# Performance work log

Hardware: AMD Instinct MI355X
Metric: run time of the kernel (lower is better)

Reference implementation:

```python
import jax, jax.numpy as jnp
import numpy as np

NUM_HEADS = 8
GRAPH_DIM = 64
K_RATIO = 0.1
SIM_THRESH = 0.6


def _gat_layer(h_in, mask, W, a_src, a_dst, b):
    # PyG GATConv (heads=1, eval mode): lin (no bias), alpha = LeakyReLU(a_src.h_j + a_dst.h_i),
    # softmax over source nodes j per target i (edges given by dense mask, self loops included), + bias.
    h = h_in @ W                                   # [N, F]
    asrc = h @ a_src                               # [N] source term
    adst = h @ a_dst                               # [N] target term
    logits = jax.nn.leaky_relu(adst[:, None] + asrc[None, :], 0.2)  # [target i, source j]
    logits = jnp.where(mask.T, logits, -1e30)      # mask[j,i]: edge src j -> dst i (symmetric here)
    alpha = jax.nn.softmax(logits, axis=-1)
    return alpha @ h + b


def _forward(x, w_qkv, w_proj, b_proj, gat0_W, gat0_asrc, gat0_adst, gat0_b,
             gat1_W, gat1_asrc, gat1_adst, gat1_b, w_g2a, b_g2a):
    B, C, H, W = x.shape
    HW = H * W
    nh = NUM_HEADS
    hd = C // nh
    scale = hd ** -0.5
    x_seq = x.reshape(B, C, HW).transpose(0, 2, 1)                 # [B, HW, C]

    # ---- build_spatial_graph ----
    importance = jnp.var(x_seq, axis=-1, ddof=1)                   # torch.var default unbiased
    N = int(HW * K_RATIO)                                          # 102 nodes
    _, top_idx = jax.lax.top_k(importance, N)                      # [B, N]
    feats = jnp.take_along_axis(x_seq, top_idx[..., None], axis=1) # [B, N, C]
    fn = feats / jnp.clip(jnp.linalg.norm(feats, axis=-1, keepdims=True), 1e-12)
    sim = fn @ fn.transpose(0, 2, 1)                               # [B, N, N]
    adj = sim > SIM_THRESH
    adj = adj | jnp.eye(N, dtype=bool)                             # GATConv add_self_loops

    # ---- per-batch GAT stack + graph_to_attn ----
    def per_graph(f, m):
        g = jax.nn.relu(_gat_layer(f, m, gat0_W, gat0_asrc, gat0_adst, gat0_b))
        g = jax.nn.relu(_gat_layer(g, m, gat1_W, gat1_asrc, gat1_adst, gat1_b))
        return jax.nn.sigmoid(g @ w_g2a.T + b_g2a)                 # [N, nh]
    gw = jax.vmap(per_graph)(feats, adj)                           # [B, N, nh]

    # ---- dense multi-head attention ----
    qkv = (x_seq @ w_qkv.T).reshape(B, HW, 3, nh, hd).transpose(2, 0, 3, 1, 4)
    q, k, v = qkv[0], qkv[1], qkv[2]                               # [B, nh, HW, hd]
    scores = jnp.einsum('bhqd,bhkd->bhqk', q, k) * scale           # [B, nh, HW, HW]

    # ---- graph modulation scatter (replaces the nested python loops) ----
    vals = jnp.where(adj[..., None], gw[:, :, None, :] * gw[:, None, :, :], 0.0)  # [B, N, N, nh]
    gm = jnp.zeros_like(scores)
    bidx = jnp.arange(B)[:, None, None]
    gm = gm.at[bidx, :, top_idx[:, :, None], top_idx[:, None, :]].set(vals)
    scores = scores + gm

    attn = jax.nn.softmax(scores, axis=-1)                         # dropout is identity in eval
    out = jnp.einsum('bhqk,bhkd->bhqd', attn, v).transpose(0, 2, 1, 3).reshape(B, HW, C)
    out = out @ w_proj.T + b_proj
    return out.transpose(0, 2, 1).reshape(B, C, H, W)


def setup_inputs() -> dict:
    key = jax.random.key(0)
    ks = jax.random.split(key, 16)
    dim, gd, nh = 256, GRAPH_DIM, NUM_HEADS
    B, H, W = 8, 32, 32
    s = 0.02
    return {
        'x': jax.random.normal(ks[0], (B, dim, H, W), dtype=jnp.float32),
        'w_qkv': s * jax.random.normal(ks[1], (3 * dim, dim), dtype=jnp.float32),
        'w_proj': s * jax.random.normal(ks[2], (dim, dim), dtype=jnp.float32),
        'b_proj': jnp.zeros((dim,), dtype=jnp.float32),
        'gat0_W': s * jax.random.normal(ks[3], (dim, gd), dtype=jnp.float32),
        'gat0_asrc': s * jax.random.normal(ks[4], (gd,), dtype=jnp.float32),
        'gat0_adst': s * jax.random.normal(ks[5], (gd,), dtype=jnp.float32),
        'gat0_b': jnp.zeros((gd,), dtype=jnp.float32),
        'gat1_W': s * jax.random.normal(ks[6], (gd, gd), dtype=jnp.float32),
        'gat1_asrc': s * jax.random.normal(ks[7], (gd,), dtype=jnp.float32),
        'gat1_adst': s * jax.random.normal(ks[8], (gd,), dtype=jnp.float32),
        'gat1_b': jnp.zeros((gd,), dtype=jnp.float32),
        'w_g2a': s * jax.random.normal(ks[9], (nh, gd), dtype=jnp.float32),
        'b_g2a': jnp.zeros((nh,), dtype=jnp.float32),
    }


def reference(x, w_qkv, w_proj, b_proj, gat0_W, gat0_asrc, gat0_adst, gat0_b,
              gat1_W, gat1_asrc, gat1_adst, gat1_b, w_g2a, b_g2a):
    return _forward(x, w_qkv, w_proj, b_proj, gat0_W, gat0_asrc, gat0_adst, gat0_b,
                    gat1_W, gat1_asrc, gat1_adst, gat1_b, w_g2a, b_g2a)
```

## Files before the change

kernel.cpp:

```cpp
#include <hip/hip_runtime.h>
#include <math.h>

#define NB 8
#define CDIM 256
#define HWD 1024
#define NH 8
#define HD 32
#define NN 102
#define GD 64

typedef __attribute__((ext_vector_type(8))) short bf16x8;
typedef __attribute__((ext_vector_type(4))) float f32x4;

__device__ inline short f2bf(float f) {
  union { float f; unsigned u; } v; v.f = f;
  unsigned r = v.u + 0x7fffu + ((v.u >> 16) & 1u);
  return (short)(r >> 16);
}
__device__ inline float bf2f(short s) {
  union { unsigned u; float f; } v;
  v.u = ((unsigned)(unsigned short)s) << 16;
  return v.f;
}

__global__ __launch_bounds__(256) void wsplitprep_k(const float* __restrict__ w_qkv,
                                                    const float* __restrict__ w_proj,
                                                    const float* __restrict__ g0W,
                                                    const float* __restrict__ g1W,
                                                    short* __restrict__ wqh, short* __restrict__ wql,
                                                    short* __restrict__ wph, short* __restrict__ wpl,
                                                    short* __restrict__ w0bT,
                                                    short* __restrict__ w1bT) {
  int bx = blockIdx.x;
  if (bx < 1024) {
    int t = bx * 256 + threadIdx.x;
    if (t < 196608) {
      float v = w_qkv[t];
      short hi = f2bf(v);
      wqh[t] = hi; wql[t] = f2bf(v - bf2f(hi));
    } else {
      int u = t - 196608;
      float v = w_proj[u];
      short hi = f2bf(v);
      wph[u] = hi; wpl[u] = f2bf(v - bf2f(hi));
    }
  } else {
    int t = (bx - 1024) * 256 + threadIdx.x;
    if (t < 16384) {
      int c = t >> 6, f = t & 63;
      w0bT[f * 256 + c] = f2bf(g0W[t]);
    } else if (t < 20480) {
      int u2 = t - 16384;
      int c = u2 >> 6, f = u2 & 63;
      w1bT[f * 64 + c] = f2bf(g1W[u2]);
    }
  }
}

__global__ __launch_bounds__(256) void xsplit_k(const float* __restrict__ x,
                                                short* __restrict__ xth,
                                                short* __restrict__ xtl) {
  __shared__ float tile[64][65];
  int p0 = blockIdx.x * 64, c0 = blockIdx.y * 64, b = blockIdx.z;
  int t = threadIdx.x;
  {
    int g = t >> 6, p = t & 63;
#pragma unroll
    for (int i = 0; i < 16; ++i) {
      int cc = g * 16 + i;
      tile[cc][p] = x[((size_t)(b * 256 + c0 + cc)) * 1024 + p0 + p];
    }
  }
  __syncthreads();
  {
    int p = t >> 2, cs = (t & 3) * 16;
    size_t rb = ((size_t)(b * 1024 + p0 + p)) * 256 + c0 + cs;
#pragma unroll
    for (int g = 0; g < 4; ++g) {
      short4 hv, lv;
      float f0 = tile[cs + g * 4 + 0][p];
      float f1 = tile[cs + g * 4 + 1][p];
      float f2 = tile[cs + g * 4 + 2][p];
      float f3 = tile[cs + g * 4 + 3][p];
      hv.x = f2bf(f0); lv.x = f2bf(f0 - bf2f(hv.x));
      hv.y = f2bf(f1); lv.y = f2bf(f1 - bf2f(hv.y));
      hv.z = f2bf(f2); lv.z = f2bf(f2 - bf2f(hv.z));
      hv.w = f2bf(f3); lv.w = f2bf(f3 - bf2f(hv.w));
      *(short4*)(xth + rb + g * 4) = hv;
      *(short4*)(xtl + rb + g * 4) = lv;
    }
  }
}

__global__ __launch_bounds__(256) void importance_k(const float* __restrict__ x,
                                                    float* __restrict__ imp) {
  __shared__ float red[8][33];
  int bp = blockIdx.x;
  int b = bp >> 5, p0 = (bp & 31) << 5;
  int t = threadIdx.x;
  int pl = t & 31, cg = t >> 5;
  const float* xp = x + (size_t)b * CDIM * HWD + p0 + pl;
  float s = 0.f;
  for (int cc = 0; cc < 32; ++cc) s += xp[(size_t)(cg * 32 + cc) * HWD];
  red[cg][pl] = s;
  __syncthreads();
  float tot = 0.f;
  for (int g = 0; g < 8; ++g) tot += red[g][pl];
  float mean = tot * (1.f / CDIM);
  __syncthreads();
  float v = 0.f;
  for (int cc = 0; cc < 32; ++cc) {
    float d = xp[(size_t)(cg * 32 + cc) * HWD] - mean;
    v += d * d;
  }
  red[cg][pl] = v;
  __syncthreads();
  if (t < 32) {
    float vv = 0.f;
    for (int g = 0; g < 8; ++g) vv += red[g][t];
    imp[b * 1024 + p0 + t] = vv * (1.f / (CDIM - 1));
  }
}

union GraphLDS {
  struct { float sv[1024]; int si[1024]; } tk;
  short featsB[NN * 264];
  struct { short alphaB[NN * 136]; short gB[NN * 72]; } ly;
};

__global__ __launch_bounds__(1024) void graph_k(
    const float* __restrict__ imp,
    const short* __restrict__ xth, const short* __restrict__ xtl,
    const short* __restrict__ w0bT, const short* __restrict__ w1bT,
    const float* __restrict__ g0as, const float* __restrict__ g0ad,
    const float* __restrict__ g0b,
    const float* __restrict__ g1as, const float* __restrict__ g1ad,
    const float* __restrict__ g1b,
    const float* __restrict__ wg2a, const float* __restrict__ bg2a,
    short* __restrict__ h0tG,
    float* __restrict__ gwp,
    unsigned long long* __restrict__ posadj)
{
  __shared__ GraphLDS u;
  __shared__ ushort adjPack[NN][8];
  __shared__ float rnL[NN];
  __shared__ float asrcL[112], adstL[112];
  __shared__ int topiL[NN];
  __shared__ int nodeofL[1024];
  int b = blockIdx.x, t = threadIdx.x;
  int wv = t >> 6, lane = t & 63, quad = lane >> 4, l16 = lane & 15;
  short* hb = h0tG + (size_t)b * 64 * 128;

  u.tk.sv[t] = imp[b * 1024 + t];
  u.tk.si[t] = t;
  nodeofL[t] = -1;
  for (int e = t; e < 64 * 26; e += 1024) hb[(e / 26) * 128 + 102 + (e % 26)] = 0;
  __syncthreads();
  for (int k = 2; k <= 1024; k <<= 1) {
    for (int j = k >> 1; j > 0; j >>= 1) {
      int ixj = t ^ j;
      if (ixj > t) {
        bool up = ((t & k) == 0);
        float a = u.tk.sv[t], c = u.tk.sv[ixj];
        if ((a > c) == up) {
          u.tk.sv[t] = c; u.tk.sv[ixj] = a;
          int ti = u.tk.si[t]; u.tk.si[t] = u.tk.si[ixj]; u.tk.si[ixj] = ti;
        }
      }
      __syncthreads();
    }
  }
  if (t >= 1024 - NN) {
    int n = 1023 - t;
    int idx = u.tk.si[t];
    topiL[n] = idx;
    nodeofL[idx] = n;
  }
  __syncthreads();

  {
    int n = t >> 3, g = t & 7;
    if (n < NN) {
      int p = topiL[n];
      const short* xh = xth + ((size_t)(b * 1024 + p)) * 256 + g * 32;
      const short* xl = xtl + ((size_t)(b * 1024 + p)) * 256 + g * 32;
      float ss = 0.f;
#pragma unroll
      for (int c8 = 0; c8 < 4; ++c8) {
        bf16x8 hv = *(const bf16x8*)(xh + c8 * 8);
        bf16x8 lv = *(const bf16x8*)(xl + c8 * 8);
#pragma unroll
        for (int j = 0; j < 8; ++j) {
          float f = bf2f(hv[j]) + bf2f(lv[j]);
          ss += f * f;
        }
        *(bf16x8*)(&u.featsB[n * 264 + g * 32 + c8 * 8]) = hv;
      }
      ss += __shfl_xor(ss, 1);
      ss += __shfl_xor(ss, 2);
      ss += __shfl_xor(ss, 4);
      if (g == 0) rnL[n] = 1.f / fmaxf(sqrtf(ss), 1e-12f);
    }
  }
  __syncthreads();

  for (int tile = wv; tile < 49; tile += 16) {
    int I = tile / 7, J = tile % 7;
    int rA = I * 16 + l16; if (rA > NN - 1) rA = NN - 1;
    int rB = J * 16 + l16; if (rB > NN - 1) rB = NN - 1;
    const short* ap = &u.featsB[rA * 264 + quad * 8];
    const short* bp = &u.featsB[rB * 264 + quad * 8];
    f32x4 acc = (f32x4){0.f, 0.f, 0.f, 0.f};
#pragma unroll
    for (int kb = 0; kb < 8; ++kb)
      acc = __builtin_amdgcn_mfma_f32_16x16x32_bf16(*(const bf16x8*)(ap + kb * 32),
                                                    *(const bf16x8*)(bp + kb * 32), acc, 0, 0, 0);
#pragma unroll
    for (int r = 0; r < 4; ++r) {
      int i = I * 16 + quad * 4 + r, j = J * 16 + l16;
      bool e = (i < NN && j < NN) &&
               ((acc[r] * rnL[i < NN ? i : 0] * rnL[j < NN ? j : 0] > 0.6f) || (i == j));
      unsigned long long m = __ballot(e);
      if (l16 == 0 && i < NN) adjPack[i][J] = (ushort)((m >> (quad * 16)) & 0xFFFFull);
    }
  }
  __syncthreads();

  if (wv < 7) {
    int mt = wv;
    int ar = mt * 16 + l16; if (ar > NN - 1) ar = NN - 1;
    const short* ap = &u.featsB[ar * 264 + quad * 8];
    float s1[4] = {0.f, 0.f, 0.f, 0.f}, s2[4] = {0.f, 0.f, 0.f, 0.f};
#pragma unroll
    for (int nt = 0; nt < 4; ++nt) {
      const short* bp = w0bT + (nt * 16 + l16) * 256 + quad * 8;
      f32x4 acc = (f32x4){0.f, 0.f, 0.f, 0.f};
#pragma unroll
      for (int kb = 0; kb < 8; ++kb)
        acc = __builtin_amdgcn_mfma_f32_16x16x32_bf16(*(const bf16x8*)(ap + kb * 32),
                                                      *(const bf16x8*)(bp + kb * 32), acc, 0, 0, 0);
      int f = nt * 16 + l16;
      float a_s = g0as[f], a_d = g0ad[f];
#pragma unroll
      for (int r = 0; r < 4; ++r) {
        int node = mt * 16 + quad * 4 + r;
        if (node < NN) hb[f * 128 + node] = f2bf(acc[r]);
        s1[r] += acc[r] * a_s;
        s2[r] += acc[r] * a_d;
      }
    }
#pragma unroll
    for (int r = 0; r < 4; ++r) {
      float v1 = s1[r], v2 = s2[r];
      v1 += __shfl_xor(v1, 1); v1 += __shfl_xor(v1, 2);
      v1 += __shfl_xor(v1, 4); v1 += __shfl_xor(v1, 8);
      v2 += __shfl_xor(v2, 1); v2 += __shfl_xor(v2, 2);
      v2 += __shfl_xor(v2, 4); v2 += __shfl_xor(v2, 8);
      int node = mt * 16 + quad * 4 + r;
      if (l16 == 0 && node < NN) { asrcL[node] = v1; adstL[node] = v2; }
    }
  }
  __syncthreads();

  for (int layer = 0; layer < 2; ++layer) {
    for (int i = wv; i < NN; i += 16) {
      float zi = adstL[i];
      int j1 = 64 + lane;
      bool e0 = (adjPack[i][lane >> 4] >> (lane & 15)) & 1;
      bool e1 = (j1 < NN) && ((adjPack[i][j1 >> 4] >> (j1 & 15)) & 1);
      float p0 = 0.f, p1 = 0.f;
      if (e0) { float z = zi + asrcL[lane]; p0 = __expf(z > 0.f ? z : 0.2f * z); }
      if (e1) { float z = zi + asrcL[j1]; p1 = __expf(z > 0.f ? z : 0.2f * z); }
      float s = p0 + p1;
      s += __shfl_xor(s, 1); s += __shfl_xor(s, 2); s += __shfl_xor(s, 4);
      s += __shfl_xor(s, 8); s += __shfl_xor(s, 16); s += __shfl_xor(s, 32);
      float inv = 1.f / s;
      u.ly.alphaB[i * 136 + lane] = f2bf(p0 * inv);
      u.ly.alphaB[i * 136 + 64 + lane] = f2bf(p1 * inv);
    }
    __syncthreads();
    {
      const float* bias = layer ? g1b : g0b;
      for (int tile = wv; tile < 28; tile += 16) {
        int mt = tile >> 2, nt = tile & 3;
        int ar = mt * 16 + l16; if (ar > NN - 1) ar = NN - 1;
        const short* ap = &u.ly.alphaB[ar * 136 + quad * 8];
        const short* bp = hb + (nt * 16 + l16) * 128 + quad * 8;
        f32x4 acc = (f32x4){0.f, 0.f, 0.f, 0.f};
#pragma unroll
        for (int kb = 0; kb < 4; ++kb)
          acc = __builtin_amdgcn_mfma_f32_16x16x32_bf16(*(const bf16x8*)(ap + kb * 32),
                                                        *(const bf16x8*)(bp + kb * 32), acc, 0, 0, 0);
        int f = nt * 16 + l16;
        float bv = bias[f];
#pragma unroll
        for (int r = 0; r < 4; ++r) {
          int i = mt * 16 + quad * 4 + r;
          if (i < NN) u.ly.gB[i * 72 + f] = f2bf(fmaxf(acc[r] + bv, 0.f));
        }
      }
    }
    __syncthreads();
    if (layer == 0) {
      if (wv < 7) {
        int mt = wv;
        int ar = mt * 16 + l16; if (ar > NN - 1) ar = NN - 1;
        const short* ap = &u.ly.gB[ar * 72 + quad * 8];
        float s1[4] = {0.f, 0.f, 0.f, 0.f}, s2[4] = {0.f, 0.f, 0.f, 0.f};
#pragma unroll
        for (int nt = 0; nt < 4; ++nt) {
          const short* bp = w1bT + (nt * 16 + l16) * 64 + quad * 8;
          f32x4 acc = (f32x4){0.f, 0.f, 0.f, 0.f};
#pragma unroll
          for (int kb = 0; kb < 2; ++kb)
            acc = __builtin_amdgcn_mfma_f32_16x16x32_bf16(*(const bf16x8*)(ap + kb * 32),
                                                          *(const bf16x8*)(bp + kb * 32), acc, 0, 0, 0);
          int f = nt * 16 + l16;
          float a_s = g1as[f], a_d = g1ad[f];
#pragma unroll
          for (int r = 0; r < 4; ++r) {
            int node = mt * 16 + quad * 4 + r;
            if (node < NN) hb[f * 128 + node] = f2bf(acc[r]);
            s1[r] += acc[r] * a_s;
            s2[r] += acc[r] * a_d;
          }
        }
#pragma unroll
        for (int r = 0; r < 4; ++r) {
          float v1 = s1[r], v2 = s2[r];
          v1 += __shfl_xor(v1, 1); v1 += __shfl_xor(v1, 2);
          v1 += __shfl_xor(v1, 4); v1 += __shfl_xor(v1, 8);
          v2 += __shfl_xor(v2, 1); v2 += __shfl_xor(v2, 2);
          v2 += __shfl_xor(v2, 4); v2 += __shfl_xor(v2, 8);
          int node = mt * 16 + quad * 4 + r;
          if (l16 == 0 && node < NN) { asrcL[node] = v1; adstL[node] = v2; }
        }
      }
      __syncthreads();
    }
  }

  float* wgL = (float*)&u.ly.alphaB[0];
  float* gwN = wgL + 512;
  if (t < 512) wgL[t] = wg2a[t];
  __syncthreads();
  if (t < NN * NH) {
    int n = t >> 3, h = t & 7;
    float z = bg2a[h];
#pragma unroll
    for (int c = 0; c < GD; ++c) z += bf2f(u.ly.gB[n * 72 + c]) * wgL[h * 64 + c];
    gwN[n * 8 + h] = 1.f / (1.f + __expf(-z));
  }
  __syncthreads();

  {
    int p = t;
    int n = nodeofL[p];
#pragma unroll
    for (int h = 0; h < 8; ++h)
      gwp[(size_t)(b * 8 + h) * 1024 + p] = (n >= 0) ? gwN[n * 8 + h] : 0.f;
    unsigned long long m[16];
#pragma unroll
    for (int w = 0; w < 16; ++w) m[w] = 0;
    if (n >= 0) {
      for (int w = 0; w < 7; ++w) {
        unsigned bits = adjPack[n][w];
        while (bits) {
          int j = __ffs(bits) - 1;
          int pj = topiL[w * 16 + j];
          m[pj >> 6] |= 1ull << (pj & 63);
          bits &= bits - 1;
        }
      }
    }
#pragma unroll
    for (int w = 0; w < 16; ++w)
      posadj[((size_t)b * 16 + w) * 1024 + p] = m[w];
  }
}

__global__ __launch_bounds__(256, 4) void qkv_k(const short* __restrict__ xth,
                                                const short* __restrict__ xtl,
                                                const short* __restrict__ wqh,
                                                const short* __restrict__ wql,
                                                short* __restrict__ qhp, short* __restrict__ qlp,
                                                short* __restrict__ khp, short* __restrict__ klp,
                                                short* __restrict__ vtp) {
  __shared__ short st_s[4][16 * 40 * 2];
  int t = threadIdx.x, wid = t >> 6, lane = t & 63, quad = lane >> 4, l16 = lane & 15;
  int m0 = blockIdx.x * 64, y = blockIdx.y;
  int b = m0 >> 10;
  int row = m0 + wid * 16 + l16;
  int p_base = (m0 & 1023) + wid * 16;
  int qi = y >> 3, n0 = (y & 7) * 32;
  const short* wh = wqh + ((size_t)qi * 256 + n0) * 256;
  const short* wl = wql + ((size_t)qi * 256 + n0) * 256;
  const short* arh = xth + (size_t)row * 256 + quad * 8;
  const short* arl = xtl + (size_t)row * 256 + quad * 8;
  f32x4 acc[2];
  acc[0] = (f32x4){0.f, 0.f, 0.f, 0.f};
  acc[1] = (f32x4){0.f, 0.f, 0.f, 0.f};
#pragma unroll
  for (int kb = 0; kb < 8; ++kb) {
    bf16x8 ah = *(const bf16x8*)(arh + kb * 32);
    bf16x8 al = *(const bf16x8*)(arl + kb * 32);
#pragma unroll
    for (int nt = 0; nt < 2; ++nt) {
      size_t wo = (size_t)(nt * 16 + l16) * 256 + kb * 32 + quad * 8;
      bf16x8 bh_ = *(const bf16x8*)(wh + wo);
      bf16x8 bl_ = *(const bf16x8*)(wl + wo);
      acc[nt] = __builtin_amdgcn_mfma_f32_16x16x32_bf16(ah, bh_, acc[nt], 0, 0, 0);
      acc[nt] = __builtin_amdgcn_mfma_f32_16x16x32_bf16(ah, bl_, acc[nt], 0, 0, 0);
      acc[nt] = __builtin_amdgcn_mfma_f32_16x16x32_bf16(al, bh_, acc[nt], 0, 0, 0);
    }
  }
  int h = n0 >> 5;
  if (qi < 2) {
    const float scale = (qi == 0) ? 0.17677669529663687f : 1.f;
    short* hp = (qi == 0) ? qhp : khp;
    short* lp = (qi == 0) ? qlp : klp;
    short* vsh = &st_s[wid][0];
    short* vsl = &st_s[wid][640];
#pragma unroll
    for (int nt = 0; nt < 2; ++nt) {
      int d = nt * 16 + l16;
#pragma unroll
      for (int r = 0; r < 4; ++r) {
        float v = acc[nt][r] * scale;
        short hi = f2bf(v);
        vsh[(quad * 4 + r) * 40 + d] = hi;
        vsl[(quad * 4 + r) * 40 + d] = f2bf(v - bf2f(hi));
      }
    }
    int orow = lane >> 2, seg = lane & 3;
    size_t e = ((size_t)(b * 8 + h) * 1024 + p_base + orow) * 32 + seg * 8;
    *(bf16x8*)(hp + e) = *(const bf16x8*)(vsh + orow * 40 + seg * 8);
    *(bf16x8*)(lp + e) = *(const bf16x8*)(vsl + orow * 40 + seg * 8);
  } else {
    short* vsv = &st_s[0][0];
#pragma unroll
    for (int nt = 0; nt < 2; ++nt) {
      int d = nt * 16 + l16;
#pragma unroll
      for (int r = 0; r < 4; ++r)
        vsv[d * 72 + (quad * 4 + r) * 4 + wid] = f2bf(acc[nt][r]);
    }
    __syncthreads();
    int d = t >> 3, g = t & 7;
    size_t rb = ((size_t)(b * 8 + h) * 32 + d) * 1024 + (m0 & 1023) + g * 8;
    *(bf16x8*)(vtp + rb) = *(const bf16x8*)(vsv + d * 72 + g * 8);
  }
}

__global__ __launch_bounds__(256, 4) void attn_k(const short* __restrict__ qh,
                                                 const short* __restrict__ ql,
                                                 const short* __restrict__ kh,
                                                 const short* __restrict__ kl,
                                                 const short* __restrict__ vt,
                                                 const float* __restrict__ gwp,
                                                 const unsigned long long* __restrict__ posadj,
                                                 short* __restrict__ aoh,
                                                 short* __restrict__ aol) {
  __shared__ __align__(16) short p_s[4][16 * 72];
  __shared__ float aw_s[4][16];
  int t = threadIdx.x;
  int wid = t >> 6, lane = t & 63, quad = lane >> 4, l16 = lane & 15;
  int bh = blockIdx.x, b = bh >> 3, h = bh & 7;
  int q0 = blockIdx.y * 64 + wid * 16;
  size_t base = (size_t)bh * 32768;
  short* pw = &p_s[wid][0];
  float* aw = &aw_s[wid][0];

  size_t qoff = base + (size_t)(q0 + l16) * 32 + quad * 8;
  bf16x8 qhf = *(const bf16x8*)(qh + qoff);
  bf16x8 qlf = *(const bf16x8*)(ql + qoff);

  const float* gwpBH = gwp + (size_t)bh * 1024;
  const unsigned long long* paB = posadj + (size_t)b * 16 * 1024;
  float grq[4];
#pragma unroll
  for (int r = 0; r < 4; ++r) grq[r] = gwpBH[q0 + quad * 4 + r];

  f32x4 ot[2];
  ot[0] = (f32x4){0.f, 0.f, 0.f, 0.f};
  ot[1] = (f32x4){0.f, 0.f, 0.f, 0.f};
  float l_r[4] = {0.f, 0.f, 0.f, 0.f};

  for (int ch = 0; ch < 16; ++ch) {
    int c0 = ch * 64;
    bf16x8 khf[4], klf[4];
#pragma unroll
    for (int ni = 0; ni < 4; ++ni) {
      size_t off = base + (size_t)(c0 + ni * 16 + l16) * 32 + quad * 8;
      khf[ni] = *(const bf16x8*)(kh + off);
      klf[ni] = *(const bf16x8*)(kl + off);
    }
    bf16x8 vaf[2][2];
#pragma unroll
    for (int mi = 0; mi < 2; ++mi)
#pragma unroll
      for (int ks = 0; ks < 2; ++ks)
        vaf[mi][ks] = *(const bf16x8*)(vt + base + (size_t)(mi * 16 + l16) * 1024 +
                                       c0 + ks * 32 + quad * 8);
    float gc[4];
#pragma unroll
    for (int ni = 0; ni < 4; ++ni) gc[ni] = gwpBH[c0 + ni * 16 + l16];
    unsigned long long mr[4];
#pragma unroll
    for (int r = 0; r < 4; ++r)
      mr[r] = paB[(size_t)ch * 1024 + q0 + quad * 4 + r];
    f32x4 s[4];
#pragma unroll
    for (int ni = 0; ni < 4; ++ni) {
      f32x4 a = (f32x4){0.f, 0.f, 0.f, 0.f};
      a = __builtin_amdgcn_mfma_f32_16x16x32_bf16(qhf, khf[ni], a, 0, 0, 0);
      a = __builtin_amdgcn_mfma_f32_16x16x32_bf16(qhf, klf[ni], a, 0, 0, 0);
      a = __builtin_amdgcn_mfma_f32_16x16x32_bf16(qlf, khf[ni], a, 0, 0, 0);
      s[ni] = a;
    }
#pragma unroll
    for (int r = 0; r < 4; ++r) {
#pragma unroll
      for (int ni = 0; ni < 4; ++ni) {
        bool bit = (mr[r] >> (ni * 16 + l16)) & 1ull;
        s[ni][r] += bit ? grq[r] * gc[ni] : 0.f;
      }
    }
#pragma unroll
    for (int r = 0; r < 4; ++r) {
      float e0 = __expf(s[0][r]);
      float e1 = __expf(s[1][r]);
      float e2 = __expf(s[2][r]);
      float e3 = __expf(s[3][r]);
      l_r[r] += (e0 + e1) + (e2 + e3);
      short4 pq = {f2bf(e0), f2bf(e1), f2bf(e2), f2bf(e3)};
      *(short4*)(pw + (quad * 4 + r) * 72 + l16 * 4) = pq;
    }
#pragma unroll
    for (int ks = 0; ks < 2; ++ks) {
      bf16x8 pb = *(const bf16x8*)(pw + l16 * 72 + ks * 32 + quad * 8);
      ot[0] = __builtin_amdgcn_mfma_f32_16x16x32_bf16(vaf[0][ks], pb, ot[0], 0, 0, 0);
      ot[1] = __builtin_amdgcn_mfma_f32_16x16x32_bf16(vaf[1][ks], pb, ot[1], 0, 0, 0);
    }
  }
#pragma unroll
  for (int r = 0; r < 4; ++r) {
    float ls = l_r[r];
    ls += __shfl_xor(ls, 1);
    ls += __shfl_xor(ls, 2);
    ls += __shfl_xor(ls, 4);
    ls += __shfl_xor(ls, 8);
    if (l16 == 0) aw[quad * 4 + r] = 1.f / ls;
  }
  float li = aw[l16];
  ot[0] *= li;
  ot[1] *= li;
  float* os = (float*)pw;
#pragma unroll
  for (int mi = 0; mi < 2; ++mi)
#pragma unroll
    for (int r = 0; r < 4; ++r)
      os[l16 * 36 + mi * 16 + quad * 4 + r] = ot[mi][r];
  int qr2 = lane >> 2, dg = (lane & 3) * 8;
  float f[8];
  *(float4*)&f[0] = *(float4*)&os[qr2 * 36 + dg];
  *(float4*)&f[4] = *(float4*)&os[qr2 * 36 + dg + 4];
  bf16x8 hv, lv;
#pragma unroll
  for (int j = 0; j < 8; ++j) {
    hv[j] = f2bf(f[j]);
    lv[j] = f2bf(f[j] - bf2f(hv[j]));
  }
  size_t ob = (size_t)(b * 1024 + q0 + qr2) * 256 + h * 32 + dg;
  *(bf16x8*)(aoh + ob) = hv;
  *(bf16x8*)(aol + ob) = lv;
}

__global__ __launch_bounds__(256, 4) void proj_k(const short* __restrict__ aoh,
                                                 const short* __restrict__ aol,
                                                 const short* __restrict__ wph,
                                                 const short* __restrict__ wpl,
                                                 const float* __restrict__ bias,
                                                 float* __restrict__ out) {
  __shared__ float os_s[4][32 * 20];
  int t = threadIdx.x, wid = t >> 6, lane = t & 63, quad = lane >> 4, l16 = lane & 15;
  int m0 = blockIdx.x * 64, n0 = blockIdx.y * 32;
  int b = m0 >> 10;
  int row = m0 + wid * 16 + l16;
  int p_base = (m0 & 1023) + wid * 16;
  const short* arh = aoh + (size_t)row * 256 + quad * 8;
  const short* arl = aol + (size_t)row * 256 + quad * 8;
  f32x4 acc[2];
  acc[0] = (f32x4){0.f, 0.f, 0.f, 0.f};
  acc[1] = (f32x4){0.f, 0.f, 0.f, 0.f};
#pragma unroll
  for (int kb = 0; kb < 8; ++kb) {
    bf16x8 ah = *(const bf16x8*)(arh + kb * 32);
    bf16x8 al = *(const bf16x8*)(arl + kb * 32);
#pragma unroll
    for (int nt = 0; nt < 2; ++nt) {
      size_t wo = (size_t)(n0 + nt * 16 + l16) * 256 + kb * 32 + quad * 8;
      bf16x8 bh_ = *(const bf16x8*)(wph + wo);
      bf16x8 bl_ = *(const bf16x8*)(wpl + wo);
      acc[nt] = __builtin_amdgcn_mfma_f32_16x16x32_bf16(ah, bh_, acc[nt], 0, 0, 0);
      acc[nt] = __builtin_amdgcn_mfma_f32_16x16x32_bf16(ah, bl_, acc[nt], 0, 0, 0);
      acc[nt] = __builtin_amdgcn_mfma_f32_16x16x32_bf16(al, bh_, acc[nt], 0, 0, 0);
    }
  }
  float* os = &os_s[wid][0];
#pragma unroll
  for (int nt = 0; nt < 2; ++nt) {
    float bv = bias[n0 + nt * 16 + l16];
#pragma unroll
    for (int r = 0; r < 4; ++r)
      os[(nt * 16 + l16) * 20 + quad * 4 + r] = acc[nt][r] + bv;
  }
  int cl = lane >> 1, hf = lane & 1;
  int c = n0 + cl;
  float* orow = out + ((size_t)(b * 256 + c)) * 1024 + p_base;
  *(float4*)(orow + hf * 8) = *(float4*)&os[cl * 20 + hf * 8];
  *(float4*)(orow + hf * 8 + 4) = *(float4*)&os[cl * 20 + hf * 8 + 4];
}

extern "C" void kernel_launch(void* const* d_in, const int* in_sizes, int n_in,
                              void* d_out, int out_size, void* d_ws, size_t ws_size,
                              hipStream_t stream) {
  const float* x      = (const float*)d_in[0];
  const float* w_qkv  = (const float*)d_in[1];
  const float* w_proj = (const float*)d_in[2];
  const float* b_proj = (const float*)d_in[3];
  const float* g0W    = (const float*)d_in[4];
  const float* g0as   = (const float*)d_in[5];
  const float* g0ad   = (const float*)d_in[6];
  const float* g0b    = (const float*)d_in[7];
  const float* g1W    = (const float*)d_in[8];
  const float* g1as   = (const float*)d_in[9];
  const float* g1ad   = (const float*)d_in[10];
  const float* g1b    = (const float*)d_in[11];
  const float* wg2a   = (const float*)d_in[12];
  const float* bg2a   = (const float*)d_in[13];
  float* out = (float*)d_out;
  float* ws = (float*)d_ws;

  size_t o = 0;
  auto alloc = [&](size_t nf) { float* p = ws + o; o += (nf + 15) & ~(size_t)15; return p; };
  float* imp    = alloc(8 * 1024);
  short* w0bT   = (short*)alloc(256 * 64 / 2);
  short* w1bT   = (short*)alloc(64 * 64 / 2);
  short* h0tG   = (short*)alloc(8 * 64 * 128 / 2);
  float* gwp    = alloc(64 * 1024);
  unsigned long long* posadj = (unsigned long long*)alloc(8 * 16 * 1024 * 2);
  short* xth    = (short*)alloc(1048576);
  short* xtl    = (short*)alloc(1048576);
  short* wqh    = (short*)alloc(98304);
  short* wql    = (short*)alloc(98304);
  short* wph    = (short*)alloc(32768);
  short* wpl    = (short*)alloc(32768);
  short* qh     = (short*)alloc(1048576);
  short* ql     = (short*)alloc(1048576);
  short* kh     = (short*)alloc(1048576);
  short* kl     = (short*)alloc(1048576);
  short* vt     = (short*)alloc(1048576);
  short* aoh    = (short*)alloc(1048576);
  short* aol    = (short*)alloc(1048576);
  if (ws_size < o * sizeof(float)) return;

  importance_k<<<256, 256, 0, stream>>>(x, imp);
  wsplitprep_k<<<1104, 256, 0, stream>>>(w_qkv, w_proj, g0W, g1W,
                                         wqh, wql, wph, wpl, w0bT, w1bT);
  xsplit_k<<<dim3(16, 4, 8), 256, 0, stream>>>(x, xth, xtl);
  graph_k<<<8, 1024, 0, stream>>>(imp, xth, xtl, w0bT, w1bT,
                                  g0as, g0ad, g0b, g1as, g1ad, g1b,
                                  wg2a, bg2a, h0tG, gwp, posadj);
  qkv_k<<<dim3(128, 24), 256, 0, stream>>>(xth, xtl, wqh, wql, qh, ql, kh, kl, vt);
  attn_k<<<dim3(64, 16), 256, 0, stream>>>(qh, ql, kh, kl, vt, gwp, posadj, aoh, aol);
  proj_k<<<dim3(128, 8), 256, 0, stream>>>(aoh, aol, wph, wpl, b_proj, out);
}
```

Baseline: 300.9 us.

## Double-buffer 32-key attention chunks and fold log2e into scale for exp2

The attention loop moves from 16 chunks of 64 keys to 32 chunks of 32 keys. Each next chunk's K, V, gate and mask loads are issued before the current chunk's compute, using register double buffering so load latency overlaps the MFMAs. The Q scale and the graph gate weights are pre-multiplied by log2(e) so the softmax can use exp2f instead of __expf. The V transpose staging layout in qkv_k changes to match the 32-key fragments, and an extra scaled gate buffer is written by graph_k. The cost is more register pressure from the buffered fragments and a second gate array.

```diff
diff --git a/kernel.cpp b/kernel.cpp
--- a/kernel.cpp
+++ b/kernel.cpp
@@ -139,6 +139,7 @@
     const float* __restrict__ wg2a, const float* __restrict__ bg2a,
     short* __restrict__ h0tG,
     float* __restrict__ gwp,
+    float* __restrict__ gwp2,
     unsigned long long* __restrict__ posadj)
 {
   __shared__ GraphLDS u;
@@ -357,8 +358,11 @@
     int p = t;
     int n = nodeofL[p];
 #pragma unroll
-    for (int h = 0; h < 8; ++h)
-      gwp[(size_t)(b * 8 + h) * 1024 + p] = (n >= 0) ? gwN[n * 8 + h] : 0.f;
+    for (int h = 0; h < 8; ++h) {
+      float g = (n >= 0) ? gwN[n * 8 + h] : 0.f;
+      gwp[(size_t)(b * 8 + h) * 1024 + p] = g;
+      gwp2[(size_t)(b * 8 + h) * 1024 + p] = g * 1.4426950408889634f;
+    }
     unsigned long long m[16];
 #pragma unroll
     for (int w = 0; w < 16; ++w) m[w] = 0;
@@ -416,7 +420,7 @@
   }
   int h = n0 >> 5;
   if (qi < 2) {
-    const float scale = (qi == 0) ? 0.17677669529663687f : 1.f;
+    const float scale = (qi == 0) ? 0.2550348595158156f : 1.f;
     short* hp = (qi == 0) ? qhp : khp;
     short* lp = (qi == 0) ? qlp : klp;
     short* vsh = &st_s[wid][0];
@@ -443,7 +447,7 @@
       int d = nt * 16 + l16;
 #pragma unroll
       for (int r = 0; r < 4; ++r)
-        vsv[d * 72 + (quad * 4 + r) * 4 + wid] = f2bf(acc[nt][r]);
+        vsv[d * 72 + (quad * 4 + r) * 2 + (wid & 1) + (wid >> 1) * 32] = f2bf(acc[nt][r]);
     }
     __syncthreads();
     int d = t >> 3, g = t & 7;
@@ -458,6 +462,7 @@
                                                  const short* __restrict__ kl,
                                                  const short* __restrict__ vt,
                                                  const float* __restrict__ gwp,
+                                                 const float* __restrict__ gwp2,
                                                  const unsigned long long* __restrict__ posadj,
                                                  short* __restrict__ aoh,
                                                  short* __restrict__ aol) {
@@ -476,73 +481,77 @@
   bf16x8 qlf = *(const bf16x8*)(ql + qoff);
 
   const float* gwpBH = gwp + (size_t)bh * 1024;
-  const unsigned long long* paB = posadj + (size_t)b * 16 * 1024;
+  const float* gwp2BH = gwp2 + (size_t)bh * 1024;
+  const unsigned* pa32 = (const unsigned*)(posadj + (size_t)b * 16 * 1024);
   float grq[4];
 #pragma unroll
-  for (int r = 0; r < 4; ++r) grq[r] = gwpBH[q0 + quad * 4 + r];
+  for (int r = 0; r < 4; ++r) grq[r] = gwp2BH[q0 + quad * 4 + r];
 
   f32x4 ot[2];
   ot[0] = (f32x4){0.f, 0.f, 0.f, 0.f};
   ot[1] = (f32x4){0.f, 0.f, 0.f, 0.f};
   float l_r[4] = {0.f, 0.f, 0.f, 0.f};
 
-  for (int ch = 0; ch < 16; ++ch) {
-    int c0 = ch * 64;
-    bf16x8 khf[4], klf[4];
-#pragma unroll
-    for (int ni = 0; ni < 4; ++ni) {
-      size_t off = base + (size_t)(c0 + ni * 16 + l16) * 32 + quad * 8;
-      khf[ni] = *(const bf16x8*)(kh + off);
-      klf[ni] = *(const bf16x8*)(kl + off);
-    }
-    bf16x8 vaf[2][2];
-#pragma unroll
-    for (int mi = 0; mi < 2; ++mi)
-#pragma unroll
-      for (int ks = 0; ks < 2; ++ks)
-        vaf[mi][ks] = *(const bf16x8*)(vt + base + (size_t)(mi * 16 + l16) * 1024 +
-                                       c0 + ks * 32 + quad * 8);
-    float gc[4];
-#pragma unroll
-    for (int ni = 0; ni < 4; ++ni) gc[ni] = gwpBH[c0 + ni * 16 + l16];
-    unsigned long long mr[4];
-#pragma unroll
-    for (int r = 0; r < 4; ++r)
-      mr[r] = paB[(size_t)ch * 1024 + q0 + quad * 4 + r];
-    f32x4 s[4];
-#pragma unroll
-    for (int ni = 0; ni < 4; ++ni) {
+  bf16x8 khb[2][2], klb[2][2], vab[2][2];
+  float gcb[2][2];
+  unsigned mrb[2][4];
+
+#define LOADCHUNK(pa_, ch_)                                                        \
+  {                                                                                \
+    int c0_ = (ch_) * 32;                                                          \
+    _Pragma("unroll")                                                              \
+    for (int ni = 0; ni < 2; ++ni) {                                               \
+      size_t off_ = base + (size_t)(c0_ + ni * 16 + l16) * 32 + quad * 8;          \
+      khb[pa_][ni] = *(const bf16x8*)(kh + off_);                                  \
+      klb[pa_][ni] = *(const bf16x8*)(kl + off_);                                  \
+      gcb[pa_][ni] = gwpBH[c0_ + ni * 16 + l16];                                   \
+    }                                                                              \
+    _Pragma("unroll")                                                              \
+    for (int mi = 0; mi < 2; ++mi)                                                 \
+      vab[pa_][mi] = *(const bf16x8*)(vt + base + (size_t)(mi * 16 + l16) * 1024 + \
+                                      c0_ + quad * 8);                             \
+    _Pragma("unroll")                                                              \
+    for (int r = 0; r < 4; ++r)                                                    \
+      mrb[pa_][r] = pa32[(((size_t)((ch_) >> 1) * 1024) + q0 + quad * 4 + r) * 2 + \
+                         ((ch_) & 1)];                                             \
+  }
+
+  LOADCHUNK(0, 0)
+#pragma unroll 2
+  for (int ch = 0; ch < 32; ++ch) {
+    int pa = ch & 1;
+    if (ch < 31) LOADCHUNK(!pa, ch + 1)
+    f32x4 s[2];
+#pragma unroll
+    for (int ni = 0; ni < 2; ++ni) {
       f32x4 a = (f32x4){0.f, 0.f, 0.f, 0.f};
-      a = __builtin_amdgcn_mfma_f32_16x16x32_bf16(qhf, khf[ni], a, 0, 0, 0);
-      a = __builtin_amdgcn_mfma_f32_16x16x32_bf16(qhf, klf[ni], a, 0, 0, 0);
-      a = __builtin_amdgcn_mfma_f32_16x16x32_bf16(qlf, khf[ni], a, 0, 0, 0);
+      a = __builtin_amdgcn_mfma_f32_16x16x32_bf16(qhf, khb[pa][ni], a, 0, 0, 0);
+      a = __builtin_amdgcn_mfma_f32_16x16x32_bf16(qhf, klb[pa][ni], a, 0, 0, 0);
+      a = __builtin_amdgcn_mfma_f32_16x16x32_bf16(qlf, khb[pa][ni], a, 0, 0, 0);
       s[ni] = a;
     }
 #pragma unroll
     for (int r = 0; r < 4; ++r) {
 #pragma unroll
-      for (int ni = 0; ni < 4; ++ni) {
-        bool bit = (mr[r] >> (ni * 16 + l16)) & 1ull;
-        s[ni][r] += bit ? grq[r] * gc[ni] : 0.f;
+      for (int ni = 0; ni < 2; ++ni) {
+        bool bit = (mrb[pa][r] >> (ni * 16 + l16)) & 1u;
+        s[ni][r] += bit ? grq[r] * gcb[pa][ni] : 0.f;
       }
     }
 #pragma unroll
     for (int r = 0; r < 4; ++r) {
-      float e0 = __expf(s[0][r]);
-      float e1 = __expf(s[1][r]);
-      float e2 = __expf(s[2][r]);
-      float e3 = __expf(s[3][r]);
-      l_r[r] += (e0 + e1) + (e2 + e3);
-      short4 pq = {f2bf(e0), f2bf(e1), f2bf(e2), f2bf(e3)};
-      *(short4*)(pw + (quad * 4 + r) * 72 + l16 * 4) = pq;
-    }
-#pragma unroll
-    for (int ks = 0; ks < 2; ++ks) {
-      bf16x8 pb = *(const bf16x8*)(pw + l16 * 72 + ks * 32 + quad * 8);
-      ot[0] = __builtin_amdgcn_mfma_f32_16x16x32_bf16(vaf[0][ks], pb, ot[0], 0, 0, 0);
-      ot[1] = __builtin_amdgcn_mfma_f32_16x16x32_bf16(vaf[1][ks], pb, ot[1], 0, 0, 0);
-    }
-  }
+      float e0 = exp2f(s[0][r]);
+      float e1 = exp2f(s[1][r]);
+      l_r[r] += e0 + e1;
+      short2 pq = {f2bf(e0), f2bf(e1)};
+      *(short2*)(pw + (quad * 4 + r) * 40 + l16 * 2) = pq;
+    }
+    bf16x8 pb = *(const bf16x8*)(pw + l16 * 40 + quad * 8);
+    ot[0] = __builtin_amdgcn_mfma_f32_16x16x32_bf16(vab[pa][0], pb, ot[0], 0, 0, 0);
+    ot[1] = __builtin_amdgcn_mfma_f32_16x16x32_bf16(vab[pa][1], pb, ot[1], 0, 0, 0);
+  }
+#undef LOADCHUNK
+
 #pragma unroll
   for (int r = 0; r < 4; ++r) {
     float ls = l_r[r];
@@ -649,6 +658,7 @@
   short* w1bT   = (short*)alloc(64 * 64 / 2);
   short* h0tG   = (short*)alloc(8 * 64 * 128 / 2);
   float* gwp    = alloc(64 * 1024);
+  float* gwp2   = alloc(64 * 1024);
   unsigned long long* posadj = (unsigned long long*)alloc(8 * 16 * 1024 * 2);
   short* xth    = (short*)alloc(1048576);
   short* xtl    = (short*)alloc(1048576);
@@ -671,8 +681,8 @@
   xsplit_k<<<dim3(16, 4, 8), 256, 0, stream>>>(x, xth, xtl);
   graph_k<<<8, 1024, 0, stream>>>(imp, xth, xtl, w0bT, w1bT,
                                   g0as, g0ad, g0b, g1as, g1ad, g1b,
-                                  wg2a, bg2a, h0tG, gwp, posadj);
+                                  wg2a, bg2a, h0tG, gwp, gwp2, posadj);
   qkv_k<<<dim3(128, 24), 256, 0, stream>>>(xth, xtl, wqh, wql, qh, ql, kh, kl, vt);
-  attn_k<<<dim3(64, 16), 256, 0, stream>>>(qh, ql, kh, kl, vt, gwp, posadj, aoh, aol);
+  attn_k<<<dim3(64, 16), 256, 0, stream>>>(qh, ql, kh, kl, vt, gwp, gwp2, posadj, aoh, aol);
   proj_k<<<dim3(128, 8), 256, 0, stream>>>(aoh, aol, wph, wpl, b_proj, out);
 }
```

New measurement: 383.8 us. 1.28x slower.
